# Kernel tuning notes

Hardware: AMD Instinct MI355X
Metric: run time of the kernel (lower is better)

## Reference

```python
import jax, jax.numpy as jnp
import numpy as np

B, L, D, K = 64, 200, 256, 8
EPS = 1e-5
SCALE = 1.0 / float(np.sqrt(D))


def _ln(x, g, b):
    mu = jnp.mean(x, -1, keepdims=True)
    var = jnp.mean((x - mu) ** 2, -1, keepdims=True)
    return (x - mu) * jax.lax.rsqrt(var + EPS) * g + b


def setup_inputs() -> dict:
    key = jax.random.key(0)
    ks = jax.random.split(key, 20)
    inp = {
        "local_item_emb": jax.random.normal(ks[0], (B, L, D), jnp.float32),
        "global_item_emb": jax.random.normal(ks[1], (B, L, D), jnp.float32),
        "intentions": jax.random.normal(ks[2], (K, D), jnp.float32),
        "pos_fai": jax.random.normal(ks[3], (L, D), jnp.float32),  # max_len == L here
        "rou": jax.random.normal(ks[4], (D,), jnp.float32),
        "W_w": jax.random.normal(ks[5], (D, D), jnp.float32) * 0.05,
        "W_b": jnp.zeros((D,), jnp.float32),
    }
    for i in range(1, 6):  # 5 LayerNorms, slightly perturbed affines
        inp[f"g{i}"] = 1.0 + 0.1 * jax.random.normal(ks[5 + i], (D,), jnp.float32)
        inp[f"b{i}"] = 0.1 * jax.random.normal(ks[10 + i], (D,), jnp.float32)
    inp["seq_len"] = jax.random.randint(ks[16], (B,), 1, L + 1)  # valid lengths in [1, L]
    return inp


def reference(local_item_emb, global_item_emb, intentions, pos_fai, rou, W_w, W_b,
              g1, b1, g2, b2, g3, b3, g4, b4, g5, b5, seq_len):
    b = local_item_emb.shape[0]

    def disen(item_emb):
        # item -> intention score [B, L, K]
        score = jax.nn.softmax(
            jnp.einsum("bld,kd->blk", _ln(item_emb, g1, b1), _ln(intentions, g2, b2)) * SCALE,
            axis=-1)
        # last-valid-token attention weight [B, L]
        idx = seq_len - 1
        q_row = item_emb[jnp.arange(b), idx] + pos_fai[idx] + rou  # [B, D]
        q = _ln(q_row, g3, b3)
        key_hat = _ln(item_emb + pos_fai[None, :item_emb.shape[1]], g4, b4)
        keyv = key_hat + jax.nn.relu(key_hat @ W_w.T + W_b)
        w = jax.nn.softmax(jnp.einsum("bd,bld->bl", q, keyv) * SCALE, axis=-1)
        # fuse scores and broadcast-multiply into [B, K, L, D]
        fuse = (score * w[..., None]).transpose(0, 2, 1)[..., None]  # [B, K, L, 1]
        return _ln(fuse * item_emb[:, None], g5, b5)

    return disen(local_item_emb) + disen(global_item_emb)
```

## Files before the change

kernel.cpp:

```cpp
#include <hip/hip_runtime.h>

#define Bn 64
#define Ln 200
#define Dn 256
#define Kn 8
#define LPn 208
#define EPSf 1e-5f
#define SCALEf 0.0625f

typedef short bf16x8 __attribute__((ext_vector_type(8)));
typedef float f32x4  __attribute__((ext_vector_type(4)));

__device__ __forceinline__ unsigned short f2bf(float f) {
    unsigned int u = __builtin_bit_cast(unsigned int, f);
    u += 0x7fffu + ((u >> 16) & 1u);
    return (unsigned short)(u >> 16);
}

__device__ __forceinline__ float wsum(float v) {
    v += __shfl_xor(v, 32, 64);
    v += __shfl_xor(v, 16, 64);
    v += __shfl_xor(v, 8, 64);
    v += __shfl_xor(v, 4, 64);
    v += __shfl_xor(v, 2, 64);
    v += __shfl_xor(v, 1, 64);
    return v;
}

__global__ __launch_bounds__(256) void kprep(
    const float* __restrict__ intentions, const float* __restrict__ g2, const float* __restrict__ b2,
    const float* __restrict__ loc, const float* __restrict__ glob,
    const float* __restrict__ pos, const float* __restrict__ rou,
    const float* __restrict__ g3, const float* __restrict__ b3,
    const int*   __restrict__ seq_len, const float* __restrict__ Ww,
    float* __restrict__ i2hat, float* __restrict__ q, unsigned short* __restrict__ wfrag)
{
    int blk = blockIdx.x, tid = threadIdx.x;
    int lane = tid & 63;
    if (blk < 2) {
        int k = blk * 4 + (tid >> 6);
        const float4 x4 = *(const float4*)(intentions + k * Dn + lane * 4);
        float x[4] = {x4.x, x4.y, x4.z, x4.w};
        float s1 = x[0] + x[1] + x[2] + x[3];
        float s2 = x[0]*x[0] + x[1]*x[1] + x[2]*x[2] + x[3]*x[3];
        s1 = wsum(s1); s2 = wsum(s2);
        float mu = s1 * (1.0f / Dn);
        float var = s2 * (1.0f / Dn) - mu * mu;
        float rs = rsqrtf(var + EPSf);
        const float4 gg = *(const float4*)(g2 + lane * 4);
        const float4 bb = *(const float4*)(b2 + lane * 4);
        float4 o;
        o.x = (x[0]-mu)*rs*gg.x + bb.x; o.y = (x[1]-mu)*rs*gg.y + bb.y;
        o.z = (x[2]-mu)*rs*gg.z + bb.z; o.w = (x[3]-mu)*rs*gg.w + bb.w;
        *(float4*)(i2hat + k * Dn + lane * 4) = o;
    } else if (blk < 34) {
        int wid = (blk - 2) * 4 + (tid >> 6);
        int s = wid / Bn, b = wid % Bn;
        const float* item = s ? glob : loc;
        int idx = seq_len[b] - 1;
        const float4 x4 = *(const float4*)(item + (b * Ln + idx) * Dn + lane * 4);
        const float4 p4 = *(const float4*)(pos + idx * Dn + lane * 4);
        const float4 r4 = *(const float4*)(rou + lane * 4);
        float x[4] = {x4.x + p4.x + r4.x, x4.y + p4.y + r4.y,
                      x4.z + p4.z + r4.z, x4.w + p4.w + r4.w};
        float s1 = x[0] + x[1] + x[2] + x[3];
        float s2 = x[0]*x[0] + x[1]*x[1] + x[2]*x[2] + x[3]*x[3];
        s1 = wsum(s1); s2 = wsum(s2);
        float mu = s1 * (1.0f / Dn);
        float var = s2 * (1.0f / Dn) - mu * mu;
        float rs = rsqrtf(var + EPSf);
        const float4 gg = *(const float4*)(g3 + lane * 4);
        const float4 bb = *(const float4*)(b3 + lane * 4);
        float4 o;
        o.x = (x[0]-mu)*rs*gg.x + bb.x; o.y = (x[1]-mu)*rs*gg.y + bb.y;
        o.z = (x[2]-mu)*rs*gg.z + bb.z; o.w = (x[3]-mu)*rs*gg.w + bb.w;
        *(float4*)(q + wid * Dn + lane * 4) = o;
    } else {
        int gt = (blk - 34) * 256 + tid;
        int frag = gt >> 6, fl = gt & 63;
        int kt = frag >> 4, nt = frag & 15;
        int d = nt * 16 + (fl & 15);
        int e = kt * 32 + (fl >> 4) * 8;
        const float* src = Ww + d * Dn + e;
        unsigned short tmp[8];
#pragma unroll
        for (int j = 0; j < 8; ++j) tmp[j] = f2bf(src[j]);
        ushort4 lo, hi;
        lo.x = tmp[0]; lo.y = tmp[1]; lo.z = tmp[2]; lo.w = tmp[3];
        hi.x = tmp[4]; hi.y = tmp[5]; hi.z = tmp[6]; hi.w = tmp[7];
        unsigned short* dst = wfrag + (size_t)gt * 8;
        *(ushort4*)(dst) = lo;
        *(ushort4*)(dst + 4) = hi;
    }
}

__global__ __launch_bounds__(256) void krow(
    const float* __restrict__ loc, const float* __restrict__ glob, const float* __restrict__ pos,
    const float* __restrict__ g1, const float* __restrict__ b1,
    const float* __restrict__ g4, const float* __restrict__ b4,
    const float* __restrict__ i2hat, const float* __restrict__ q,
    float* __restrict__ score, float* __restrict__ stats, float* __restrict__ qkh,
    unsigned short* __restrict__ kh16)
{
    int wid = blockIdx.x * 4 + (threadIdx.x >> 6);
    int lane = threadIdx.x & 63;
    int s = wid / (Bn * LPn);
    int rem = wid % (Bn * LPn);
    int b = rem / LPn, l = rem % LPn;
    unsigned short* khrow = kh16 + ((size_t)(s * Bn + b) * LPn + l) * Dn;
    if (l >= Ln) {
        ushort4 z; z.x = z.y = z.z = z.w = 0;
        *(ushort4*)(khrow + lane * 4) = z;
        return;
    }
    const float* item = s ? glob : loc;
    const float4 x4 = *(const float4*)(item + ((size_t)(b * Ln + l)) * Dn + lane * 4);
    const float4 p4 = *(const float4*)(pos + l * Dn + lane * 4);
    float x[4] = {x4.x, x4.y, x4.z, x4.w};
    float p[4] = {p4.x, p4.y, p4.z, p4.w};

    float s1 = x[0] + x[1] + x[2] + x[3];
    float s2 = x[0]*x[0] + x[1]*x[1] + x[2]*x[2] + x[3]*x[3];
#pragma unroll
    for (int m = 32; m >= 1; m >>= 1) { s1 += __shfl_xor(s1, m, 64); s2 += __shfl_xor(s2, m, 64); }
    float mu = s1 * (1.0f / Dn);
    float var = s2 * (1.0f / Dn) - mu * mu;
    float rs = rsqrtf(var + EPSf);

    const float4 gg1 = *(const float4*)(g1 + lane * 4);
    const float4 bb1 = *(const float4*)(b1 + lane * 4);
    float x1[4];
    x1[0] = (x[0]-mu)*rs*gg1.x + bb1.x; x1[1] = (x[1]-mu)*rs*gg1.y + bb1.y;
    x1[2] = (x[2]-mu)*rs*gg1.z + bb1.z; x1[3] = (x[3]-mu)*rs*gg1.w + bb1.w;

    float lg[Kn];
#pragma unroll
    for (int k = 0; k < Kn; ++k) {
        const float4 iv = *(const float4*)(i2hat + k * Dn + lane * 4);
        float pk = x1[0]*iv.x + x1[1]*iv.y + x1[2]*iv.z + x1[3]*iv.w;
        lg[k] = wsum(pk);
    }
    float mx = -1e30f;
#pragma unroll
    for (int k = 0; k < Kn; ++k) { lg[k] *= SCALEf; mx = fmaxf(mx, lg[k]); }
    float se = 0.f;
    float ex[Kn];
#pragma unroll
    for (int k = 0; k < Kn; ++k) { ex[k] = __expf(lg[k] - mx); se += ex[k]; }
    float inv = 1.0f / se;
    int r = (s * Bn + b) * Ln + l;
    if (lane < Kn) score[(size_t)r * Kn + lane] = ex[lane] * inv;
    if (lane == 0) { stats[2 * (size_t)r] = mu; stats[2 * (size_t)r + 1] = var; }

    float y[4] = {x[0]+p[0], x[1]+p[1], x[2]+p[2], x[3]+p[3]};
    float t1 = y[0] + y[1] + y[2] + y[3];
    float t2 = y[0]*y[0] + y[1]*y[1] + y[2]*y[2] + y[3]*y[3];
#pragma unroll
    for (int m = 32; m >= 1; m >>= 1) { t1 += __shfl_xor(t1, m, 64); t2 += __shfl_xor(t2, m, 64); }
    float muy = t1 * (1.0f / Dn);
    float vay = t2 * (1.0f / Dn) - muy * muy;
    float rsy = rsqrtf(vay + EPSf);
    const float4 gg4 = *(const float4*)(g4 + lane * 4);
    const float4 bb4 = *(const float4*)(b4 + lane * 4);
    float kh[4];
    kh[0] = (y[0]-muy)*rsy*gg4.x + bb4.x; kh[1] = (y[1]-muy)*rsy*gg4.y + bb4.y;
    kh[2] = (y[2]-muy)*rsy*gg4.z + bb4.z; kh[3] = (y[3]-muy)*rsy*gg4.w + bb4.w;
    ushort4 kv;
    kv.x = f2bf(kh[0]); kv.y = f2bf(kh[1]); kv.z = f2bf(kh[2]); kv.w = f2bf(kh[3]);
    *(ushort4*)(khrow + lane * 4) = kv;

    const float4 qv = *(const float4*)(q + (size_t)(s * Bn + b) * Dn + lane * 4);
    float pq = kh[0]*qv.x + kh[1]*qv.y + kh[2]*qv.z + kh[3]*qv.w;
    pq = wsum(pq);
    if (lane == 0) qkh[r] = pq;
}

__global__ __launch_bounds__(256) void kgemm(
    const unsigned short* __restrict__ kh16, const unsigned short* __restrict__ wfrag,
    const float* __restrict__ q, const float* __restrict__ Wb,
    const float* __restrict__ qkh, float* __restrict__ wlogit)
{
    int blk = blockIdx.x;
    int sb = blk / 13, mt = blk % 13;
    int wv = threadIdx.x >> 6, lane = threadIdx.x & 63;

    f32x4 acc[4];
#pragma unroll
    for (int nt = 0; nt < 4; ++nt) { acc[nt][0]=0.f; acc[nt][1]=0.f; acc[nt][2]=0.f; acc[nt][3]=0.f; }

    int arow = lane & 15;
    int acol = (lane >> 4) * 8;
    const unsigned short* arowp = kh16 + ((size_t)sb * LPn + mt * 16 + arow) * Dn + acol;
    const unsigned short* bbase = wfrag + (size_t)(wv * 4) * 64 * 8 + (size_t)lane * 8;

#pragma unroll
    for (int kt = 0; kt < 8; ++kt) {
        bf16x8 af = *(const bf16x8*)(arowp + kt * 32);
#pragma unroll
        for (int nt = 0; nt < 4; ++nt) {
            bf16x8 bf = *(const bf16x8*)(bbase + ((size_t)(kt * 16 + nt) * 64) * 8);
            acc[nt] = __builtin_amdgcn_mfma_f32_16x16x32_bf16(af, bf, acc[nt], 0, 0, 0);
        }
    }

    int col = lane & 15, quad = lane >> 4;
    float qv[4], wbv[4];
#pragma unroll
    for (int nt = 0; nt < 4; ++nt) {
        int d = (wv * 4 + nt) * 16 + col;
        qv[nt] = q[(size_t)sb * Dn + d];
        wbv[nt] = Wb[d];
    }
    __shared__ float part[4][16];
#pragma unroll
    for (int j = 0; j < 4; ++j) {
        float t = 0.f;
#pragma unroll
        for (int nt = 0; nt < 4; ++nt) {
            float v = acc[nt][j] + wbv[nt];
            v = fmaxf(v, 0.f);
            t = fmaf(qv[nt], v, t);
        }
        t += __shfl_xor(t, 1, 64);
        t += __shfl_xor(t, 2, 64);
        t += __shfl_xor(t, 4, 64);
        t += __shfl_xor(t, 8, 64);
        if (col == 0) part[wv][quad * 4 + j] = t;
    }
    __syncthreads();
    int t = threadIdx.x;
    if (t < 16) {
        int l = mt * 16 + t;
        if (l < Ln)
            wlogit[(size_t)sb * Ln + l] = qkh[(size_t)sb * Ln + l]
                + part[0][t] + part[1][t] + part[2][t] + part[3][t];
    }
}

__global__ __launch_bounds__(256) void ksoft(const float* __restrict__ wlogit, float* __restrict__ wsoft)
{
    int sb = blockIdx.x, t = threadIdx.x;
    __shared__ float red[4];
    float lg = (t < Ln) ? wlogit[(size_t)sb * Ln + t] * SCALEf : -1e30f;
    float m = lg;
#pragma unroll
    for (int mk = 32; mk >= 1; mk >>= 1) m = fmaxf(m, __shfl_xor(m, mk, 64));
    if ((t & 63) == 0) red[t >> 6] = m;
    __syncthreads();
    m = fmaxf(fmaxf(red[0], red[1]), fmaxf(red[2], red[3]));
    __syncthreads();
    float ex = (t < Ln) ? __expf(lg - m) : 0.f;
    float sm = ex;
#pragma unroll
    for (int mk = 32; mk >= 1; mk >>= 1) sm += __shfl_xor(sm, mk, 64);
    if ((t & 63) == 0) red[t >> 6] = sm;
    __syncthreads();
    sm = red[0] + red[1] + red[2] + red[3];
    if (t < Ln) wsoft[(size_t)sb * Ln + t] = ex / sm;
}

__global__ __launch_bounds__(256) void kout(
    const float* __restrict__ loc, const float* __restrict__ glob,
    const float* __restrict__ score, const float* __restrict__ stats, const float* __restrict__ wsoft,
    const float* __restrict__ g5, const float* __restrict__ b5, float* __restrict__ out)
{
    int blk = blockIdx.x;
    int b = blk / Ln, l = blk % Ln;
    int d = threadIdx.x;
    size_t base = (size_t)(b * Ln + l) * Dn + d;
    float x0 = loc[base], x1 = glob[base];
    size_t r0 = (size_t)b * Ln + l;
    size_t r1 = (size_t)(Bn + b) * Ln + l;
    float mu0 = stats[2*r0], va0 = stats[2*r0+1];
    float mu1 = stats[2*r1], va1 = stats[2*r1+1];
    float w0 = wsoft[r0], w1 = wsoft[r1];
    float g5d = g5[d], b5d = b5[d];
    float dx0 = x0 - mu0, dx1 = x1 - mu1;
#pragma unroll
    for (int k = 0; k < Kn; ++k) {
        float c0 = score[r0 * Kn + k] * w0;
        float c1 = score[r1 * Kn + k] * w1;
        float a0 = c0 * rsqrtf(c0 * c0 * va0 + EPSf);
        float a1 = c1 * rsqrtf(c1 * c1 * va1 + EPSf);
        out[((size_t)(b * Kn + k) * Ln + l) * Dn + d] = g5d * (a0 * dx0 + a1 * dx1) + 2.0f * b5d;
    }
}

extern "C" void kernel_launch(void* const* d_in, const int* in_sizes, int n_in,
                              void* d_out, int out_size, void* d_ws, size_t ws_size,
                              hipStream_t stream) {
    const float* loc   = (const float*)d_in[0];
    const float* glob  = (const float*)d_in[1];
    const float* inten = (const float*)d_in[2];
    const float* pos   = (const float*)d_in[3];
    const float* rou   = (const float*)d_in[4];
    const float* Ww    = (const float*)d_in[5];
    const float* Wb    = (const float*)d_in[6];
    const float* g1 = (const float*)d_in[7],  *b1 = (const float*)d_in[8];
    const float* g2 = (const float*)d_in[9],  *b2 = (const float*)d_in[10];
    const float* g3 = (const float*)d_in[11], *b3 = (const float*)d_in[12];
    const float* g4 = (const float*)d_in[13], *b4 = (const float*)d_in[14];
    const float* g5 = (const float*)d_in[15], *b5 = (const float*)d_in[16];
    const int* seq_len = (const int*)d_in[17];
    float* out = (float*)d_out;

    char* ws = (char*)d_ws;
    size_t off = 0;
    float* i2hat = (float*)(ws + off);            off += (size_t)Kn * Dn * 4;
    float* q     = (float*)(ws + off);            off += (size_t)2 * Bn * Dn * 4;
    unsigned short* wfrag = (unsigned short*)(ws + off); off += (size_t)Dn * Dn * 2;
    unsigned short* kh16  = (unsigned short*)(ws + off); off += (size_t)2 * Bn * LPn * Dn * 2;
    float* score  = (float*)(ws + off);           off += (size_t)2 * Bn * Ln * Kn * 4;
    float* stats  = (float*)(ws + off);           off += (size_t)2 * Bn * Ln * 2 * 4;
    float* qkh    = (float*)(ws + off);           off += (size_t)2 * Bn * Ln * 4;
    float* wlogit = (float*)(ws + off);           off += (size_t)2 * Bn * Ln * 4;
    float* wsoft  = (float*)(ws + off);           off += (size_t)2 * Bn * Ln * 4;

    kprep<<<66, 256, 0, stream>>>(inten, g2, b2, loc, glob, pos, rou, g3, b3, seq_len, Ww,
                                  i2hat, q, wfrag);
    krow<<<(2 * Bn * LPn) / 4, 256, 0, stream>>>(loc, glob, pos, g1, b1, g4, b4, i2hat, q,
                                                 score, stats, qkh, kh16);
    kgemm<<<128 * 13, 256, 0, stream>>>(kh16, wfrag, q, Wb, qkh, wlogit);
    ksoft<<<2 * Bn, 256, 0, stream>>>(wlogit, wsoft);
    kout<<<Bn * Ln, 256, 0, stream>>>(loc, glob, score, stats, wsoft, g5, b5, out);
}
```

Measured before the change: 200.1 us.

## Pack rows per wave in krow, double M-tiles in kgemm, vectorize kout

```diff
diff --git a/kernel.cpp b/kernel.cpp
--- a/kernel.cpp
+++ b/kernel.cpp
@@ -4,7 +4,7 @@
 #define Ln 200
 #define Dn 256
 #define Kn 8
-#define LPn 208
+#define LPn 224
 #define EPSf 1e-5f
 #define SCALEf 0.0625f
 
@@ -24,6 +24,14 @@
     v += __shfl_xor(v, 4, 64);
     v += __shfl_xor(v, 2, 64);
     v += __shfl_xor(v, 1, 64);
+    return v;
+}
+
+__device__ __forceinline__ float gsum16(float v) {
+    v += __shfl_xor(v, 1, 64);
+    v += __shfl_xor(v, 2, 64);
+    v += __shfl_xor(v, 4, 64);
+    v += __shfl_xor(v, 8, 64);
     return v;
 }
 
@@ -102,43 +110,61 @@
     float* __restrict__ score, float* __restrict__ stats, float* __restrict__ qkh,
     unsigned short* __restrict__ kh16)
 {
-    int wid = blockIdx.x * 4 + (threadIdx.x >> 6);
+    int gw = blockIdx.x * 4 + (threadIdx.x >> 6);
     int lane = threadIdx.x & 63;
-    int s = wid / (Bn * LPn);
-    int rem = wid % (Bn * LPn);
+    int grp = lane >> 4, l16 = lane & 15;
+    int R = gw * 4 + grp;
+    int s = R / (Bn * LPn);
+    int rem = R % (Bn * LPn);
     int b = rem / LPn, l = rem % LPn;
-    unsigned short* khrow = kh16 + ((size_t)(s * Bn + b) * LPn + l) * Dn;
-    if (l >= Ln) {
-        ushort4 z; z.x = z.y = z.z = z.w = 0;
-        *(ushort4*)(khrow + lane * 4) = z;
-        return;
-    }
+    bool valid = l < Ln;
+    int lc = valid ? l : 0;
+    int doff = l16 * 16;
+
     const float* item = s ? glob : loc;
-    const float4 x4 = *(const float4*)(item + ((size_t)(b * Ln + l)) * Dn + lane * 4);
-    const float4 p4 = *(const float4*)(pos + l * Dn + lane * 4);
-    float x[4] = {x4.x, x4.y, x4.z, x4.w};
-    float p[4] = {p4.x, p4.y, p4.z, p4.w};
-
-    float s1 = x[0] + x[1] + x[2] + x[3];
-    float s2 = x[0]*x[0] + x[1]*x[1] + x[2]*x[2] + x[3]*x[3];
-#pragma unroll
-    for (int m = 32; m >= 1; m >>= 1) { s1 += __shfl_xor(s1, m, 64); s2 += __shfl_xor(s2, m, 64); }
+    const float* xrow = item + (size_t)(b * Ln + lc) * Dn + doff;
+    const float* prow = pos + (size_t)lc * Dn + doff;
+
+    float x[16], p[16];
+#pragma unroll
+    for (int v = 0; v < 4; ++v) {
+        float4 xv = *(const float4*)(xrow + v * 4);
+        float4 pv = *(const float4*)(prow + v * 4);
+        x[v*4+0] = xv.x; x[v*4+1] = xv.y; x[v*4+2] = xv.z; x[v*4+3] = xv.w;
+        p[v*4+0] = pv.x; p[v*4+1] = pv.y; p[v*4+2] = pv.z; p[v*4+3] = pv.w;
+    }
+
+    float s1 = 0.f, s2 = 0.f;
+#pragma unroll
+    for (int i = 0; i < 16; ++i) { s1 += x[i]; s2 = fmaf(x[i], x[i], s2); }
+    s1 = gsum16(s1); s2 = gsum16(s2);
     float mu = s1 * (1.0f / Dn);
     float var = s2 * (1.0f / Dn) - mu * mu;
     float rs = rsqrtf(var + EPSf);
 
-    const float4 gg1 = *(const float4*)(g1 + lane * 4);
-    const float4 bb1 = *(const float4*)(b1 + lane * 4);
-    float x1[4];
-    x1[0] = (x[0]-mu)*rs*gg1.x + bb1.x; x1[1] = (x[1]-mu)*rs*gg1.y + bb1.y;
-    x1[2] = (x[2]-mu)*rs*gg1.z + bb1.z; x1[3] = (x[3]-mu)*rs*gg1.w + bb1.w;
+    float x1[16];
+#pragma unroll
+    for (int v = 0; v < 4; ++v) {
+        float4 gg = *(const float4*)(g1 + doff + v * 4);
+        float4 bb = *(const float4*)(b1 + doff + v * 4);
+        x1[v*4+0] = (x[v*4+0]-mu)*rs*gg.x + bb.x;
+        x1[v*4+1] = (x[v*4+1]-mu)*rs*gg.y + bb.y;
+        x1[v*4+2] = (x[v*4+2]-mu)*rs*gg.z + bb.z;
+        x1[v*4+3] = (x[v*4+3]-mu)*rs*gg.w + bb.w;
+    }
 
     float lg[Kn];
 #pragma unroll
     for (int k = 0; k < Kn; ++k) {
-        const float4 iv = *(const float4*)(i2hat + k * Dn + lane * 4);
-        float pk = x1[0]*iv.x + x1[1]*iv.y + x1[2]*iv.z + x1[3]*iv.w;
-        lg[k] = wsum(pk);
+        const float* iv = i2hat + k * Dn + doff;
+        float pk = 0.f;
+#pragma unroll
+        for (int v = 0; v < 4; ++v) {
+            float4 i4 = *(const float4*)(iv + v * 4);
+            pk = fmaf(x1[v*4+0], i4.x, pk); pk = fmaf(x1[v*4+1], i4.y, pk);
+            pk = fmaf(x1[v*4+2], i4.z, pk); pk = fmaf(x1[v*4+3], i4.w, pk);
+        }
+        lg[k] = gsum16(pk);
     }
     float mx = -1e30f;
 #pragma unroll
@@ -148,31 +174,54 @@
 #pragma unroll
     for (int k = 0; k < Kn; ++k) { ex[k] = __expf(lg[k] - mx); se += ex[k]; }
     float inv = 1.0f / se;
-    int r = (s * Bn + b) * Ln + l;
-    if (lane < Kn) score[(size_t)r * Kn + lane] = ex[lane] * inv;
-    if (lane == 0) { stats[2 * (size_t)r] = mu; stats[2 * (size_t)r + 1] = var; }
-
-    float y[4] = {x[0]+p[0], x[1]+p[1], x[2]+p[2], x[3]+p[3]};
-    float t1 = y[0] + y[1] + y[2] + y[3];
-    float t2 = y[0]*y[0] + y[1]*y[1] + y[2]*y[2] + y[3]*y[3];
-#pragma unroll
-    for (int m = 32; m >= 1; m >>= 1) { t1 += __shfl_xor(t1, m, 64); t2 += __shfl_xor(t2, m, 64); }
+    size_t r = (size_t)(s * Bn + b) * Ln + l;
+    if (valid) {
+        if (l16 < Kn) score[r * Kn + l16] = ex[l16] * inv;
+        if (l16 == 0) { float2 st; st.x = mu; st.y = var; *(float2*)(stats + 2 * r) = st; }
+    }
+
+    float t1 = 0.f, t2 = 0.f;
+    float y[16];
+#pragma unroll
+    for (int i = 0; i < 16; ++i) { y[i] = x[i] + p[i]; t1 += y[i]; t2 = fmaf(y[i], y[i], t2); }
+    t1 = gsum16(t1); t2 = gsum16(t2);
     float muy = t1 * (1.0f / Dn);
     float vay = t2 * (1.0f / Dn) - muy * muy;
     float rsy = rsqrtf(vay + EPSf);
-    const float4 gg4 = *(const float4*)(g4 + lane * 4);
-    const float4 bb4 = *(const float4*)(b4 + lane * 4);
-    float kh[4];
-    kh[0] = (y[0]-muy)*rsy*gg4.x + bb4.x; kh[1] = (y[1]-muy)*rsy*gg4.y + bb4.y;
-    kh[2] = (y[2]-muy)*rsy*gg4.z + bb4.z; kh[3] = (y[3]-muy)*rsy*gg4.w + bb4.w;
-    ushort4 kv;
-    kv.x = f2bf(kh[0]); kv.y = f2bf(kh[1]); kv.z = f2bf(kh[2]); kv.w = f2bf(kh[3]);
-    *(ushort4*)(khrow + lane * 4) = kv;
-
-    const float4 qv = *(const float4*)(q + (size_t)(s * Bn + b) * Dn + lane * 4);
-    float pq = kh[0]*qv.x + kh[1]*qv.y + kh[2]*qv.z + kh[3]*qv.w;
-    pq = wsum(pq);
-    if (lane == 0) qkh[r] = pq;
+    float kh[16];
+#pragma unroll
+    for (int v = 0; v < 4; ++v) {
+        float4 gg = *(const float4*)(g4 + doff + v * 4);
+        float4 bb = *(const float4*)(b4 + doff + v * 4);
+        kh[v*4+0] = (y[v*4+0]-muy)*rsy*gg.x + bb.x;
+        kh[v*4+1] = (y[v*4+1]-muy)*rsy*gg.y + bb.y;
+        kh[v*4+2] = (y[v*4+2]-muy)*rsy*gg.z + bb.z;
+        kh[v*4+3] = (y[v*4+3]-muy)*rsy*gg.w + bb.w;
+    }
+    ushort4 kv[4];
+#pragma unroll
+    for (int v = 0; v < 4; ++v) {
+        kv[v].x = valid ? f2bf(kh[v*4+0]) : (unsigned short)0;
+        kv[v].y = valid ? f2bf(kh[v*4+1]) : (unsigned short)0;
+        kv[v].z = valid ? f2bf(kh[v*4+2]) : (unsigned short)0;
+        kv[v].w = valid ? f2bf(kh[v*4+3]) : (unsigned short)0;
+    }
+    unsigned short* khrow = kh16 + ((size_t)(s * Bn + b) * LPn + l) * Dn + doff;
+    *(ushort4*)(khrow)      = kv[0];
+    *(ushort4*)(khrow + 4)  = kv[1];
+    *(ushort4*)(khrow + 8)  = kv[2];
+    *(ushort4*)(khrow + 12) = kv[3];
+
+    const float* qrow = q + (size_t)(s * Bn + b) * Dn + doff;
+    float pq = 0.f;
+#pragma unroll
+    for (int v = 0; v < 4; ++v) {
+        float4 q4 = *(const float4*)(qrow + v * 4);
+        pq = fmaf(kh[v*4+0], q4.x, pq); pq = fmaf(kh[v*4+1], q4.y, pq);
+        pq = fmaf(kh[v*4+2], q4.z, pq); pq = fmaf(kh[v*4+3], q4.w, pq);
+    }
+    pq = gsum16(pq);
+    if (valid && l16 == 0) qkh[r] = pq;
 }
 
 __global__ __launch_bounds__(256) void kgemm(
@@ -181,25 +230,29 @@
     const float* __restrict__ qkh, float* __restrict__ wlogit)
 {
     int blk = blockIdx.x;
-    int sb = blk / 13, mt = blk % 13;
+    int sb = blk / 7, mtg = blk % 7;
     int wv = threadIdx.x >> 6, lane = threadIdx.x & 63;
 
-    f32x4 acc[4];
-#pragma unroll
-    for (int nt = 0; nt < 4; ++nt) { acc[nt][0]=0.f; acc[nt][1]=0.f; acc[nt][2]=0.f; acc[nt][3]=0.f; }
+    f32x4 acc[2][4];
+#pragma unroll
+    for (int mt = 0; mt < 2; ++mt)
+#pragma unroll
+        for (int nt = 0; nt < 4; ++nt) { acc[mt][nt][0]=0.f; acc[mt][nt][1]=0.f; acc[mt][nt][2]=0.f; acc[mt][nt][3]=0.f; }
 
     int arow = lane & 15;
     int acol = (lane >> 4) * 8;
-    const unsigned short* arowp = kh16 + ((size_t)sb * LPn + mt * 16 + arow) * Dn + acol;
+    const unsigned short* arowp = kh16 + ((size_t)sb * LPn + mtg * 32 + arow) * Dn + acol;
     const unsigned short* bbase = wfrag + (size_t)(wv * 4) * 64 * 8 + (size_t)lane * 8;
 
 #pragma unroll
     for (int kt = 0; kt < 8; ++kt) {
-        bf16x8 af = *(const bf16x8*)(arowp + kt * 32);
+        bf16x8 af0 = *(const bf16x8*)(arowp + kt * 32);
+        bf16x8 af1 = *(const bf16x8*)(arowp + 16 * Dn + kt * 32);
 #pragma unroll
         for (int nt = 0; nt < 4; ++nt) {
             bf16x8 bf = *(const bf16x8*)(bbase + ((size_t)(kt * 16 + nt) * 64) * 8);
-            acc[nt] = __builtin_amdgcn_mfma_f32_16x16x32_bf16(af, bf, acc[nt], 0, 0, 0);
+            acc[0][nt] = __builtin_amdgcn_mfma_f32_16x16x32_bf16(af0, bf, acc[0][nt], 0, 0, 0);
+            acc[1][nt] = __builtin_amdgcn_mfma_f32_16x16x32_bf16(af1, bf, acc[1][nt], 0, 0, 0);
         }
     }
 
@@ -211,26 +264,29 @@
         qv[nt] = q[(size_t)sb * Dn + d];
         wbv[nt] = Wb[d];
     }
-    __shared__ float part[4][16];
-#pragma unroll
-    for (int j = 0; j < 4; ++j) {
-        float t = 0.f;
-#pragma unroll
-        for (int nt = 0; nt < 4; ++nt) {
-            float v = acc[nt][j] + wbv[nt];
-            v = fmaxf(v, 0.f);
-            t = fmaf(qv[nt], v, t);
+    __shared__ float part[4][32];
+#pragma unroll
+    for (int mt = 0; mt < 2; ++mt) {
+#pragma unroll
+        for (int j = 0; j < 4; ++j) {
+            float t = 0.f;
+#pragma unroll
+            for (int nt = 0; nt < 4; ++nt) {
+                float v = acc[mt][nt][j] + wbv[nt];
+                v = fmaxf(v, 0.f);
+                t = fmaf(qv[nt], v, t);
+            }
+            t += __shfl_xor(t, 1, 64);
+            t += __shfl_xor(t, 2, 64);
+            t += __shfl_xor(t, 4, 64);
+            t += __shfl_xor(t, 8, 64);
+            if (col == 0) part[wv][mt * 16 + quad * 4 + j] = t;
         }
-        t += __shfl_xor(t, 1, 64);
-        t += __shfl_xor(t, 2, 64);
-        t += __shfl_xor(t, 4, 64);
-        t += __shfl_xor(t, 8, 64);
-        if (col == 0) part[wv][quad * 4 + j] = t;
     }
     __syncthreads();
     int t = threadIdx.x;
-    if (t < 16) {
-        int l = mt * 16 + t;
+    if (t < 32) {
+        int l = mtg * 32 + t;
         if (l < Ln)
             wlogit[(size_t)sb * Ln + l] = qkh[(size_t)sb * Ln + l]
                 + part[0][t] + part[1][t] + part[2][t] + part[3][t];
@@ -264,25 +320,38 @@
     const float* __restrict__ score, const float* __restrict__ stats, const float* __restrict__ wsoft,
     const float* __restrict__ g5, const float* __restrict__ b5, float* __restrict__ out)
 {
-    int blk = blockIdx.x;
-    int b = blk / Ln, l = blk % Ln;
-    int d = threadIdx.x;
-    size_t base = (size_t)(b * Ln + l) * Dn + d;
-    float x0 = loc[base], x1 = glob[base];
+    int rr = threadIdx.x >> 6;
+    int lane = threadIdx.x & 63;
+    int row = blockIdx.x * 4 + rr;
+    int b = row / Ln, l = row % Ln;
     size_t r0 = (size_t)b * Ln + l;
     size_t r1 = (size_t)(Bn + b) * Ln + l;
-    float mu0 = stats[2*r0], va0 = stats[2*r0+1];
-    float mu1 = stats[2*r1], va1 = stats[2*r1+1];
+
+    float4 x0 = *(const float4*)(loc + (size_t)row * Dn + lane * 4);
+    float4 x1 = *(const float4*)(glob + (size_t)row * Dn + lane * 4);
+    float2 st0 = *(const float2*)(stats + 2 * r0);
+    float2 st1 = *(const float2*)(stats + 2 * r1);
     float w0 = wsoft[r0], w1 = wsoft[r1];
-    float g5d = g5[d], b5d = b5[d];
-    float dx0 = x0 - mu0, dx1 = x1 - mu1;
+    float4 g5v = *(const float4*)(g5 + lane * 4);
+    float4 b5v = *(const float4*)(b5 + lane * 4);
+
+    float4 dx0, dx1;
+    dx0.x = x0.x - st0.x; dx0.y = x0.y - st0.x; dx0.z = x0.z - st0.x; dx0.w = x0.w - st0.x;
+    dx1.x = x1.x - st1.x; dx1.y = x1.y - st1.x; dx1.z = x1.z - st1.x; dx1.w = x1.w - st1.x;
+
+    float* obase = out + ((size_t)b * Kn * Ln + l) * Dn + lane * 4;
 #pragma unroll
     for (int k = 0; k < Kn; ++k) {
         float c0 = score[r0 * Kn + k] * w0;
         float c1 = score[r1 * Kn + k] * w1;
-        float a0 = c0 * rsqrtf(c0 * c0 * va0 + EPSf);
-        float a1 = c1 * rsqrtf(c1 * c1 * va1 + EPSf);
-        out[((size_t)(b * Kn + k) * Ln + l) * Dn + d] = g5d * (a0 * dx0 + a1 * dx1) + 2.0f * b5d;
+        float a0 = c0 * rsqrtf(fmaf(c0 * c0, st0.y, EPSf));
+        float a1 = c1 * rsqrtf(fmaf(c1 * c1, st1.y, EPSf));
+        float4 o;
+        o.x = fmaf(g5v.x, fmaf(a0, dx0.x, a1 * dx1.x), 2.0f * b5v.x);
+        o.y = fmaf(g5v.y, fmaf(a0, dx0.y, a1 * dx1.y), 2.0f * b5v.y);
+        o.z = fmaf(g5v.z, fmaf(a0, dx0.z, a1 * dx1.z), 2.0f * b5v.z);
+        o.w = fmaf(g5v.w, fmaf(a0, dx0.w, a1 * dx1.w), 2.0f * b5v.w);
+        *(float4*)(obase + (size_t)k * Ln * Dn) = o;
     }
 }
 
@@ -318,9 +387,9 @@
 
     kprep<<<66, 256, 0, stream>>>(inten, g2, b2, loc, glob, pos, rou, g3, b3, seq_len, Ww,
                                   i2hat, q, wfrag);
-    krow<<<(2 * Bn * LPn) / 4, 256, 0, stream>>>(loc, glob, pos, g1, b1, g4, b4, i2hat, q,
-                                                 score, stats, qkh, kh16);
-    kgemm<<<128 * 13, 256, 0, stream>>>(kh16, wfrag, q, Wb, qkh, wlogit);
+    krow<<<(2 * Bn * LPn) / 16, 256, 0, stream>>>(loc, glob, pos, g1, b1, g4, b4, i2hat, q,
+                                                  score, stats, qkh, kh16);
+    kgemm<<<128 * 7, 256, 0, stream>>>(kh16, wfrag, q, Wb, qkh, wlogit);
     ksoft<<<2 * Bn, 256, 0, stream>>>(wlogit, wsoft);
-    kout<<<Bn * Ln, 256, 0, stream>>>(loc, glob, score, stats, wsoft, g5, b5, out);
-}
+    kout<<<Bn * Ln / 4, 256, 0, stream>>>(loc, glob, score, stats, wsoft, g5, b5, out);
+}
```

New measurement: 205.9 us. 1.03x slower.
